# Optimization experiments

Measured on AMD Instinct MI355X. Metric: run time of the kernel, lower is better.

The kernel has to match this reference:

```python
import jax, jax.numpy as jnp
import numpy as np

U, I, H, E, EL = 100000, 50000, 128, 600000, 200000


def setup_inputs() -> dict:
    key = jax.random.key(0)
    ks = jax.random.split(key, 24)
    inp = {}
    inp["user_emb"] = jax.random.normal(ks[0], (U, H), jnp.float32) * 0.1
    inp["item_emb"] = jax.random.normal(ks[1], (I, H), jnp.float32) * 0.1
    s = 1.0 / np.sqrt(H)
    names = ["w1_ui_l", "w1_ui_r", "w1_iu_l", "w1_iu_r",
             "w2_ui_l", "w2_ui_r", "w2_iu_l", "w2_iu_r"]
    for i, n in enumerate(names):
        inp[n] = jax.random.uniform(ks[2 + i], (H, H), jnp.float32, -s, s)
    for i, n in enumerate(["b1_ui", "b1_iu", "b2_ui", "b2_iu"]):
        inp[n] = jax.random.uniform(ks[10 + i], (H,), jnp.float32, -s, s)
    inp["user_node_id"] = jnp.arange(U, dtype=jnp.int32)
    inp["item_node_id"] = jnp.arange(I, dtype=jnp.int32)
    src_u = jax.random.randint(ks[14], (E,), 0, U, jnp.int32)
    dst_i = jax.random.randint(ks[15], (E,), 0, I, jnp.int32)
    inp["edge_index_ui"] = jnp.stack([src_u, dst_i])  # user -> item
    inp["edge_index_iu"] = jnp.stack([dst_i, src_u])  # item -> user (reverse)
    lu = jax.random.randint(ks[16], (EL,), 0, U, jnp.int32)
    li = jax.random.randint(ks[17], (EL,), 0, I, jnp.int32)
    inp["edge_label_index"] = jnp.stack([lu, li])
    return inp


def _sage(x_src, x_dst, edge_index, w_l, b_l, w_r, num_dst):
    # PyG SAGEConv: out = lin_l(mean_j x_src[j]) + lin_r(x_dst)
    src, dst = edge_index[0], edge_index[1]
    msg = x_src[src]                                   # [E, H] gather
    agg = jax.ops.segment_sum(msg, dst, num_segments=num_dst)
    cnt = jax.ops.segment_sum(jnp.ones((msg.shape[0],), msg.dtype), dst,
                              num_segments=num_dst)
    mean = agg / jnp.maximum(cnt, 1.0)[:, None]
    return mean @ w_l + b_l + x_dst @ w_r


def reference(user_emb, item_emb,
              w1_ui_l, w1_ui_r, w1_iu_l, w1_iu_r,
              w2_ui_l, w2_ui_r, w2_iu_l, w2_iu_r,
              b1_ui, b1_iu, b2_ui, b2_iu,
              user_node_id, item_node_id,
              edge_index_ui, edge_index_iu, edge_label_index):
    xu = user_emb[user_node_id]   # [U, H]
    xi = item_emb[item_node_id]   # [I, H]
    # layer 1 (hetero: each dst type aggregates from its single incoming relation)
    u1 = jax.nn.relu(_sage(xi, xu, edge_index_iu, w1_iu_l, b1_iu, w1_iu_r, U))
    i1 = jax.nn.relu(_sage(xu, xi, edge_index_ui, w1_ui_l, b1_ui, w1_ui_r, I))
    # layer 2
    u2 = _sage(i1, u1, edge_index_iu, w2_iu_l, b2_iu, w2_iu_r, U)
    i2 = _sage(u1, i1, edge_index_ui, w2_ui_l, b2_ui, w2_ui_r, I)
    # edge-indexed dot-product classifier
    fu = u2[edge_label_index[0]]  # [EL, H]
    fi = i2[edge_label_index[1]]  # [EL, H]
    return jnp.sum(fu * fi, axis=-1)
```

## Files before the change

kernel.cpp:

```cpp
#include <hip/hip_runtime.h>
#include <hip/hip_bf16.h>
#include <cstdio>

#define U_N 100000
#define I_N 50000
#define H_DIM 128
#define E_N 600000
#define EL_N 200000

#define EPB 2048
#define NBLK ((E_N + EPB - 1) / EPB)
#define SH_U 8
#define SH_I 7
#define NB_U ((U_N + 255) >> 8)
#define NB_I ((I_N + 127) >> 7)
#define LH_U (NB_U * NBLK)
#define LH_I (NB_I * NBLK)
#define LH_TOT (LH_U + LH_I)

#define CVT_BLK (((U_N + I_N) * 16) / 256)
#define PREP_BLK 512
#define NBU2 ((U_N + 255) / 256)
#define NBI2 ((I_N + 255) / 256)

typedef __attribute__((ext_vector_type(8))) short bh8;
typedef __attribute__((ext_vector_type(4))) float f32x4;
typedef __attribute__((ext_vector_type(8))) unsigned short u16x8;

__device__ inline unsigned short f2b(float f) {
  unsigned u = __builtin_bit_cast(unsigned, f);
  u += 0x7fffu + ((u >> 16) & 1u);
  return (unsigned short)(u >> 16);
}
__device__ inline float b2f(unsigned short h) {
  unsigned u = ((unsigned)h) << 16;
  return __builtin_bit_cast(float, u);
}

__global__ __launch_bounds__(256) void prep_all(
    const float* __restrict__ xu, const float* __restrict__ xi,
    const int* __restrict__ unid, const int* __restrict__ inid,
    unsigned short* __restrict__ ub, unsigned short* __restrict__ ib,
    const float* __restrict__ l0, const float* __restrict__ r0, short* __restrict__ o0,
    const float* __restrict__ l1, const float* __restrict__ r1, short* __restrict__ o1,
    const float* __restrict__ l2, const float* __restrict__ r2, short* __restrict__ o2,
    const float* __restrict__ l3, const float* __restrict__ r3, short* __restrict__ o3,
    const int* __restrict__ e_ui, int* __restrict__ hist) {
  __shared__ int h[512];
  const int b = blockIdx.x;
  const int tid = threadIdx.x;
  if (b < CVT_BLK) {
    int t = b * 256 + tid;
    const float* x;
    unsigned short* xb;
    int row, seg;
    if (t < U_N * 16) {
      row = t >> 4; seg = t & 15;
      int r0_ = row;
      row = unid ? unid[row] : row;
      x = xu; xb = ub + (size_t)r0_ * H_DIM;
    } else {
      int t2 = t - U_N * 16;
      row = t2 >> 4; seg = t2 & 15;
      int r0_ = row;
      row = inid ? inid[row] : row;
      x = xi; xb = ib + (size_t)r0_ * H_DIM;
    }
    const float* p = x + (size_t)row * H_DIM + seg * 8;
    float4 a = ((const float4*)p)[0];
    float4 c = ((const float4*)p)[1];
    u16x8 v;
    v[0] = f2b(a.x); v[1] = f2b(a.y); v[2] = f2b(a.z); v[3] = f2b(a.w);
    v[4] = f2b(c.x); v[5] = f2b(c.y); v[6] = f2b(c.z); v[7] = f2b(c.w);
    *(u16x8*)(xb + seg * 8) = v;
  } else if (b < CVT_BLK + PREP_BLK) {
    int t = (b - CVT_BLK) * 256 + tid;
    int set = t >> 15, s = t & 32767;
    const float *wl, *wr; short* W2;
    if (set == 0)      { wl = l0; wr = r0; W2 = o0; }
    else if (set == 1) { wl = l1; wr = r1; W2 = o1; }
    else if (set == 2) { wl = l2; wr = r2; W2 = o2; }
    else               { wl = l3; wr = r3; W2 = o3; }
    int col = s >> 8, k = s & 255;
    float v = (k < 128) ? wl[k * 128 + col] : wr[(k - 128) * 128 + col];
    W2[col * 256 + k] = (short)f2b(v);
  } else {
    int hb = b - CVT_BLK - PREP_BLK;
    int side = hb >= NBLK;
    int blk = side ? hb - NBLK : hb;
    const int* dst = e_ui + (side ? E_N : 0);
    int shift = side ? SH_I : SH_U;
    int nbins = side ? NB_I : NB_U;
    int hbase = side ? LH_U : 0;
    for (int i = tid; i < nbins; i += 256) h[i] = 0;
    __syncthreads();
    const int base = blk * EPB;
    const int end = min(base + EPB, E_N);
    for (int i = base + tid; i < end; i += 256)
      atomicAdd(&h[((unsigned)dst[i]) >> shift], 1);
    __syncthreads();
    for (int i = tid; i < nbins; i += 256)
      hist[hbase + i * NBLK + blk] = h[i];
  }
}

__global__ __launch_bounds__(256) void scan_p1(const int* __restrict__ cnt,
                                               int* __restrict__ bsum, int n) {
  const int t = threadIdx.x;
  const int base = blockIdx.x * 1024 + t * 4;
  int s = 0;
  for (int j = 0; j < 4; ++j) {
    int i = base + j;
    if (i < n) s += cnt[i];
  }
  for (int off = 32; off > 0; off >>= 1) s += __shfl_down(s, off, 64);
  __shared__ int wsum[4];
  if ((t & 63) == 0) wsum[t >> 6] = s;
  __syncthreads();
  if (t == 0) bsum[blockIdx.x] = wsum[0] + wsum[1] + wsum[2] + wsum[3];
}

__global__ __launch_bounds__(256) void scan_p2(int* __restrict__ bsum, int nb) {
  __shared__ int sm[256];
  const int t = threadIdx.x;
  int v = (t < nb) ? bsum[t] : 0;
  sm[t] = v;
  __syncthreads();
  for (int d = 1; d < 256; d <<= 1) {
    int x = (t >= d) ? sm[t - d] : 0;
    __syncthreads();
    sm[t] += x;
    __syncthreads();
  }
  if (t < nb) bsum[t] = sm[t] - v;
}

__global__ __launch_bounds__(256) void scan_p3(const int* __restrict__ cnt,
                                               const int* __restrict__ bsum,
                                               int* __restrict__ off, int n) {
  const int t = threadIdx.x;
  const int lane = t & 63, wv = t >> 6;
  const int base = blockIdx.x * 1024 + t * 4;
  int vals[4];
  int s = 0;
  for (int j = 0; j < 4; ++j) {
    int i = base + j;
    vals[j] = (i < n) ? cnt[i] : 0;
    s += vals[j];
  }
  int inc = s;
  for (int d = 1; d < 64; d <<= 1) {
    int x = __shfl_up(inc, d, 64);
    if (lane >= d) inc += x;
  }
  __shared__ int wsum[4];
  if (lane == 63) wsum[wv] = inc;
  __syncthreads();
  int wbase = 0;
  for (int w = 0; w < wv; ++w) wbase += wsum[w];
  int excl = wbase + (inc - s) + bsum[blockIdx.x];
  for (int j = 0; j < 4; ++j) {
    int i = base + j;
    if (i < n) off[i] = excl;
    excl += vals[j];
  }
}

__global__ __launch_bounds__(256) void bin_scatter2(const int* __restrict__ e_ui,
                                                    const int* __restrict__ hoff,
                                                    unsigned* __restrict__ bucketed) {
  __shared__ int cur[512];
  const int t = threadIdx.x;
  const int hb = blockIdx.x;
  const int side = hb >= NBLK;
  const int blk = side ? hb - NBLK : hb;
  const int* dst = e_ui + (side ? E_N : 0);
  const int* src = e_ui + (side ? 0 : E_N);
  const int shift = side ? SH_I : SH_U;
  const int nbins = side ? NB_I : NB_U;
  const int hbase = side ? LH_U : 0;
  for (int i = t; i < nbins; i += 256) cur[i] = hoff[hbase + i * NBLK + blk];
  __syncthreads();
  const int base = blk * EPB;
  const int end = min(base + EPB, E_N);
  const unsigned mask = (1u << shift) - 1u;
  for (int i = base + t; i < end; i += 256) {
    unsigned d = (unsigned)dst[i];
    int bin = (int)(d >> shift);
    int pos = atomicAdd(&cur[bin], 1);
    bucketed[pos] = ((d & mask) << 24) | (unsigned)src[i];
  }
}

__global__ __launch_bounds__(256) void bin_group2(const int* __restrict__ hoff,
                                                  const unsigned* __restrict__ bucketed,
                                                  int* __restrict__ csr,
                                                  int* __restrict__ cnt_u,
                                                  int* __restrict__ off_u,
                                                  int* __restrict__ cnt_i,
                                                  int* __restrict__ off_i) {
  __shared__ int cl[256];
  __shared__ int cur[256];
  __shared__ int wsum[4];
  const int b = blockIdx.x;
  const int t = threadIdx.x;
  const int side = b >= NB_U;
  const int bb = side ? b - NB_U : b;
  const int shift = side ? SH_I : SH_U;
  const int N = side ? I_N : U_N;
  int* cnt = side ? cnt_i : cnt_u;
  int* off = side ? off_i : off_u;
  int start, end;
  if (!side) {
    start = hoff[bb * NBLK];
    end = (bb + 1 < NB_U) ? hoff[(bb + 1) * NBLK] : E_N;
  } else {
    start = hoff[LH_U + bb * NBLK];
    end = (bb + 1 < NB_I) ? hoff[LH_U + (bb + 1) * NBLK] : 2 * E_N;
  }
  const int ndst = 1 << shift;
  const int base = bb << shift;
  if (t < ndst) cl[t] = 0;
  __syncthreads();
  for (int i = start + t; i < end; i += 256)
    atomicAdd(&cl[bucketed[i] >> 24], 1);
  __syncthreads();
  int v = (t < ndst) ? cl[t] : 0;
  const int lane = t & 63, wv = t >> 6;
  int inc = v;
  for (int d = 1; d < 64; d <<= 1) {
    int x = __shfl_up(inc, d, 64);
    if (lane >= d) inc += x;
  }
  if (lane == 63) wsum[wv] = inc;
  __syncthreads();
  int wbase = 0;
  for (int q = 0; q < wv; ++q) wbase += wsum[q];
  int excl = wbase + inc - v;
  if (t < ndst) {
    cur[t] = start + excl;
    int node = base + t;
    if (node < N) { cnt[node] = v; off[node] = start + excl; }
  }
  __syncthreads();
  for (int i = start + t; i < end; i += 256) {
    unsigned w = bucketed[i];
    int pos = atomicAdd(&cur[w >> 24], 1);
    csr[pos] = (int)(w & 0xFFFFFFu);
  }
}

__global__ __launch_bounds__(256) void gather_mean2(
    const int* __restrict__ off_u, const int* __restrict__ cnt_u,
    const unsigned short* __restrict__ xsrc_u, unsigned short* __restrict__ agg_u,
    const int* __restrict__ off_i, const int* __restrict__ cnt_i,
    const unsigned short* __restrict__ xsrc_i, unsigned short* __restrict__ agg_i,
    const int* __restrict__ csr) {
  long t = (long)blockIdx.x * 256 + threadIdx.x;
  int node = (int)(t >> 4);
  int lane = (int)(t & 15);
  const int* off; const int* cnt;
  const unsigned short* xb; unsigned short* aggb;
  if (node < U_N) {
    off = off_u; cnt = cnt_u; xb = xsrc_u; aggb = agg_u;
  } else {
    node -= U_N;
    if (node >= I_N) return;
    off = off_i; cnt = cnt_i; xb = xsrc_i; aggb = agg_i;
  }
  int o = off[node], c = cnt[node];
  float acc[8] = {};
  for (int j0 = 0; j0 < c; j0 += 16) {
    int nj = c - j0;
    if (nj > 16) nj = 16;
    int sidx = (lane < nj) ? csr[o + j0 + lane] : 0;
    int j = 0;
    for (; j + 4 <= nj; j += 4) {
      u16x8 v0, v1, v2, v3;
      {
        int s0 = __shfl(sidx, j + 0, 16);
        int s1 = __shfl(sidx, j + 1, 16);
        int s2 = __shfl(sidx, j + 2, 16);
        int s3 = __shfl(sidx, j + 3, 16);
        v0 = *(const u16x8*)(xb + (size_t)s0 * H_DIM + lane * 8);
        v1 = *(const u16x8*)(xb + (size_t)s1 * H_DIM + lane * 8);
        v2 = *(const u16x8*)(xb + (size_t)s2 * H_DIM + lane * 8);
        v3 = *(const u16x8*)(xb + (size_t)s3 * H_DIM + lane * 8);
      }
      for (int k = 0; k < 8; ++k) acc[k] += b2f(v0[k]);
      for (int k = 0; k < 8; ++k) acc[k] += b2f(v1[k]);
      for (int k = 0; k < 8; ++k) acc[k] += b2f(v2[k]);
      for (int k = 0; k < 8; ++k) acc[k] += b2f(v3[k]);
    }
    for (; j < nj; ++j) {
      int s = __shfl(sidx, j, 16);
      u16x8 v = *(const u16x8*)(xb + (size_t)s * H_DIM + lane * 8);
      for (int k = 0; k < 8; ++k) acc[k] += b2f(v[k]);
    }
  }
  float inv = 1.0f / (float)(c > 0 ? c : 1);
  u16x8 r;
  for (int k = 0; k < 8; ++k) r[k] = f2b(acc[k] * inv);
  *(u16x8*)(aggb + (size_t)node * H_DIM + lane * 8) = r;
}

__global__ __launch_bounds__(256, 2) void sage_gemm2(
    const unsigned short* __restrict__ agg_u, const unsigned short* __restrict__ x_u,
    const short* __restrict__ W2_u, const float* __restrict__ bias_u,
    unsigned short* __restrict__ out_u,
    const unsigned short* __restrict__ agg_i, const unsigned short* __restrict__ x_i,
    const short* __restrict__ W2_i, const float* __restrict__ bias_i,
    unsigned short* __restrict__ out_i, int relu) {
  const unsigned short *aggb, *xb;
  const short* W2;
  const float* bias;
  unsigned short* outb;
  int N, blk;
  if (blockIdx.x < NBU2) {
    aggb = agg_u; xb = x_u; W2 = W2_u; bias = bias_u; outb = out_u;
    N = U_N; blk = blockIdx.x;
  } else {
    aggb = agg_i; xb = x_i; W2 = W2_i; bias = bias_i; outb = out_i;
    N = I_N; blk = blockIdx.x - NBU2;
  }

  __shared__ short wlds[128 * 256];
  const int tid = threadIdx.x;
  for (int c = tid; c < 4096; c += 256) {
    int col = c >> 5, g = c & 31;
    uint4 v = *(const uint4*)(W2 + col * 256 + g * 8);
    *(uint4*)(&wlds[col * 256 + ((g ^ (col & 15)) * 8)]) = v;
  }
  __syncthreads();

  const int lane = tid & 63;
  const int wave = tid >> 6;
  const int q = lane >> 4;
  const int n16 = lane & 15;
  const int rowbase = blk * 256 + wave * 64;

  const unsigned short* aptr[4];
  const unsigned short* xptr[4];
  for (int g = 0; g < 4; ++g) {
    int row = rowbase + g * 16 + n16;
    int rr = row < N ? row : 0;
    aptr[g] = aggb + (size_t)rr * H_DIM + q * 8;
    xptr[g] = xb + (size_t)rr * H_DIM + q * 8;
  }

  f32x4 acc[4][8] = {};

  for (int kt = 0; kt < 8; ++kt) {
    const int k0 = kt * 32;
    bh8 afrag[4];
    for (int g = 0; g < 4; ++g) {
      const unsigned short* p = (kt < 4) ? (aptr[g] + k0) : (xptr[g] + (k0 - 128));
      afrag[g] = *(const bh8*)(p);
    }
    const int swz = ((kt * 4 + q) ^ n16) * 8;
    for (int c = 0; c < 8; ++c) {
      bh8 b = *(const bh8*)(&wlds[(c * 16 + n16) * 256 + swz]);
      acc[0][c] = __builtin_amdgcn_mfma_f32_16x16x32_bf16(afrag[0], b, acc[0][c], 0, 0, 0);
      acc[1][c] = __builtin_amdgcn_mfma_f32_16x16x32_bf16(afrag[1], b, acc[1][c], 0, 0, 0);
      acc[2][c] = __builtin_amdgcn_mfma_f32_16x16x32_bf16(afrag[2], b, acc[2][c], 0, 0, 0);
      acc[3][c] = __builtin_amdgcn_mfma_f32_16x16x32_bf16(afrag[3], b, acc[3][c], 0, 0, 0);
    }
  }

  float bcol[8];
  for (int c = 0; c < 8; ++c) bcol[c] = bias[c * 16 + n16];

  for (int g = 0; g < 4; ++g) {
    for (int r = 0; r < 4; ++r) {
      int row = rowbase + g * 16 + q * 4 + r;
      if (row >= N) continue;
      for (int c = 0; c < 8; ++c) {
        float v = acc[g][c][r] + bcol[c];
        if (relu) v = v > 0.0f ? v : 0.0f;
        outb[(size_t)row * H_DIM + c * 16 + n16] = f2b(v);
      }
    }
  }
}

__global__ __launch_bounds__(256) void final_dot(const int* __restrict__ lbl,
                                                 const unsigned short* __restrict__ u2,
                                                 const unsigned short* __restrict__ i2,
                                                 float* __restrict__ out) {
  long t = (long)blockIdx.x * 256 + threadIdx.x;
  int e = (int)(t >> 4);
  if (e >= EL_N) return;
  int lane = (int)(t & 15);
  int lu = lbl[e];
  int li = lbl[EL_N + e];
  u16x8 a = *(const u16x8*)(u2 + (size_t)lu * H_DIM + lane * 8);
  u16x8 b = *(const u16x8*)(i2 + (size_t)li * H_DIM + lane * 8);
  float p = 0.f;
  for (int k = 0; k < 8; ++k) p += b2f(a[k]) * b2f(b[k]);
  for (int off = 8; off > 0; off >>= 1) p += __shfl_down(p, off, 16);
  if (lane == 0) out[e] = p;
}

extern "C" void kernel_launch(void* const* d_in, const int* in_sizes, int n_in,
                              void* d_out, int out_size, void* d_ws, size_t ws_size,
                              hipStream_t stream) {
  const float* user_emb = (const float*)d_in[0];
  const float* item_emb = (const float*)d_in[1];
  const float* w1_ui_l = (const float*)d_in[2];
  const float* w1_ui_r = (const float*)d_in[3];
  const float* w1_iu_l = (const float*)d_in[4];
  const float* w1_iu_r = (const float*)d_in[5];
  const float* w2_ui_l = (const float*)d_in[6];
  const float* w2_ui_r = (const float*)d_in[7];
  const float* w2_iu_l = (const float*)d_in[8];
  const float* w2_iu_r = (const float*)d_in[9];
  const float* b1_ui = (const float*)d_in[10];
  const float* b1_iu = (const float*)d_in[11];
  const float* b2_ui = (const float*)d_in[12];
  const float* b2_iu = (const float*)d_in[13];
  const int* unid = (const int*)d_in[14];
  const int* inid = (const int*)d_in[15];
  const int* e_ui = (const int*)d_in[16];
  const int* e_iu = (const int*)d_in[17];
  const int* elbl = (const int*)d_in[18];
  float* out = (float*)d_out;

  char* ws = (char*)d_ws;
  size_t o = 0;
  auto alloc = [&](size_t bytes) {
    char* p = ws + o;
    o = (o + bytes + 255) & ~(size_t)255;
    return p;
  };
  int* hist = (int*)alloc((size_t)LH_TOT * 4);
  int* hoff = (int*)alloc((size_t)LH_TOT * 4);
  unsigned* bkt = (unsigned*)alloc((size_t)2 * E_N * 4);
  int* csr = (int*)alloc((size_t)2 * E_N * 4);
  int* cnt_u = (int*)alloc((size_t)U_N * 4);
  int* cnt_i = (int*)alloc((size_t)I_N * 4);
  int* off_u = (int*)alloc((size_t)U_N * 4);
  int* off_i = (int*)alloc((size_t)I_N * 4);
  int* bsum = (int*)alloc(256 * 4);
  unsigned short* ue_b = (unsigned short*)alloc((size_t)U_N * H_DIM * 2);
  unsigned short* ie_b = (unsigned short*)alloc((size_t)I_N * H_DIM * 2);
  unsigned short* agg_u = (unsigned short*)alloc((size_t)U_N * H_DIM * 2);
  unsigned short* agg_i = (unsigned short*)alloc((size_t)I_N * H_DIM * 2);
  unsigned short* h1_u = (unsigned short*)alloc((size_t)U_N * H_DIM * 2);
  unsigned short* h1_i = (unsigned short*)alloc((size_t)I_N * H_DIM * 2);
  unsigned short* h2_u = (unsigned short*)alloc((size_t)U_N * H_DIM * 2);
  unsigned short* h2_i = (unsigned short*)alloc((size_t)I_N * H_DIM * 2);
  short* W2_1u = (short*)alloc(128 * 256 * 2);
  short* W2_1i = (short*)alloc(128 * 256 * 2);
  short* W2_2u = (short*)alloc(128 * 256 * 2);
  short* W2_2i = (short*)alloc(128 * 256 * 2);
  if (o > ws_size) {
    fprintf(stderr, "kernel_launch: ws too small, need %zu have %zu\n", o, ws_size);
    return;
  }

  prep_all<<<CVT_BLK + PREP_BLK + 2 * NBLK, 256, 0, stream>>>(
      user_emb, item_emb, unid, inid, ue_b, ie_b,
      w1_iu_l, w1_iu_r, W2_1u, w1_ui_l, w1_ui_r, W2_1i,
      w2_iu_l, w2_iu_r, W2_2u, w2_ui_l, w2_ui_r, W2_2i,
      e_ui, hist);

  const int nb1 = (LH_TOT + 1023) / 1024;
  scan_p1<<<nb1, 256, 0, stream>>>(hist, bsum, LH_TOT);
  scan_p2<<<1, 256, 0, stream>>>(bsum, nb1);
  scan_p3<<<nb1, 256, 0, stream>>>(hist, bsum, hoff, LH_TOT);

  bin_scatter2<<<2 * NBLK, 256, 0, stream>>>(e_ui, hoff, bkt);
  bin_group2<<<NB_U + NB_I, 256, 0, stream>>>(hoff, bkt, csr, cnt_u, off_u, cnt_i, off_i);

  const int g_blocks = ((U_N + I_N) * 16 + 255) / 256;
  gather_mean2<<<g_blocks, 256, 0, stream>>>(off_u, cnt_u, ie_b, agg_u,
                                             off_i, cnt_i, ue_b, agg_i, csr);
  sage_gemm2<<<NBU2 + NBI2, 256, 0, stream>>>(
      agg_u, ue_b, W2_1u, b1_iu, h1_u,
      agg_i, ie_b, W2_1i, b1_ui, h1_i, 1);

  gather_mean2<<<g_blocks, 256, 0, stream>>>(off_u, cnt_u, h1_i, agg_u,
                                             off_i, cnt_i, h1_u, agg_i, csr);
  sage_gemm2<<<NBU2 + NBI2, 256, 0, stream>>>(
      agg_u, h1_u, W2_2u, b2_iu, h2_u,
      agg_i, h1_i, W2_2i, b2_ui, h2_i, 0);

  final_dot<<<(EL_N * 16 + 255) / 256, 256, 0, stream>>>(elbl, h2_u, h2_i, out);
}
```

Baseline: 357.4 us.

## Fuse scan into single-pass chained scan; register-resident weights in SAGE GEMM

Replaces the three-kernel prefix scan with one decoupled chained-scan kernel. Each block waits on a flag/value from its predecessor, and the flags are zeroed inside prep_all. The SAGE GEMM drops its 64 KB LDS weight tile: each wave now holds its 32-column slice of the weights in registers, and every block handles 128 rows with all four waves sharing the same A rows. This removes two launches and the LDS staging and barrier, but it reloads the A fragments once per wave (4x the A global traffic). The chained scan also depends on blocks being scheduled in order for forward progress.

Measured after the change: 518.3 us. 45.0% more time.

```diff
diff --git a/kernel.cpp b/kernel.cpp
--- a/kernel.cpp
+++ b/kernel.cpp
@@ -17,11 +17,12 @@
 #define LH_U (NB_U * NBLK)
 #define LH_I (NB_I * NBLK)
 #define LH_TOT (LH_U + LH_I)
+#define SCAN_BLKS ((LH_TOT + 1023) / 1024)
 
 #define CVT_BLK (((U_N + I_N) * 16) / 256)
 #define PREP_BLK 512
-#define NBU2 ((U_N + 255) / 256)
-#define NBI2 ((I_N + 255) / 256)
+#define NBU3 ((U_N + 127) / 128)
+#define NBI3 ((I_N + 127) / 128)
 
 typedef __attribute__((ext_vector_type(8))) short bh8;
 typedef __attribute__((ext_vector_type(4))) float f32x4;
@@ -45,7 +46,7 @@
     const float* __restrict__ l1, const float* __restrict__ r1, short* __restrict__ o1,
     const float* __restrict__ l2, const float* __restrict__ r2, short* __restrict__ o2,
     const float* __restrict__ l3, const float* __restrict__ r3, short* __restrict__ o3,
-    const int* __restrict__ e_ui, int* __restrict__ hist) {
+    const int* __restrict__ e_ui, int* __restrict__ hist, int* __restrict__ fv) {
   __shared__ int h[512];
   const int b = blockIdx.x;
   const int tid = threadIdx.x;
@@ -86,6 +87,7 @@
     W2[col * 256 + k] = (short)f2b(v);
   } else {
     int hb = b - CVT_BLK - PREP_BLK;
+    if (hb == 0 && tid < SCAN_BLKS) fv[tid] = 0;
     int side = hb >= NBLK;
     int blk = side ? hb - NBLK : hb;
     const int* dst = e_ui + (side ? E_N : 0);
@@ -104,48 +106,18 @@
   }
 }
 
-__global__ __launch_bounds__(256) void scan_p1(const int* __restrict__ cnt,
-                                               int* __restrict__ bsum, int n) {
-  const int t = threadIdx.x;
-  const int base = blockIdx.x * 1024 + t * 4;
-  int s = 0;
-  for (int j = 0; j < 4; ++j) {
-    int i = base + j;
-    if (i < n) s += cnt[i];
-  }
-  for (int off = 32; off > 0; off >>= 1) s += __shfl_down(s, off, 64);
-  __shared__ int wsum[4];
-  if ((t & 63) == 0) wsum[t >> 6] = s;
-  __syncthreads();
-  if (t == 0) bsum[blockIdx.x] = wsum[0] + wsum[1] + wsum[2] + wsum[3];
-}
-
-__global__ __launch_bounds__(256) void scan_p2(int* __restrict__ bsum, int nb) {
-  __shared__ int sm[256];
-  const int t = threadIdx.x;
-  int v = (t < nb) ? bsum[t] : 0;
-  sm[t] = v;
-  __syncthreads();
-  for (int d = 1; d < 256; d <<= 1) {
-    int x = (t >= d) ? sm[t - d] : 0;
-    __syncthreads();
-    sm[t] += x;
-    __syncthreads();
-  }
-  if (t < nb) bsum[t] = sm[t] - v;
-}
-
-__global__ __launch_bounds__(256) void scan_p3(const int* __restrict__ cnt,
-                                               const int* __restrict__ bsum,
-                                               int* __restrict__ off, int n) {
+__global__ __launch_bounds__(256) void scan_chain(const int* __restrict__ hist,
+                                                  int* __restrict__ hoff,
+                                                  int* __restrict__ fv, int n) {
+  const int b = blockIdx.x;
   const int t = threadIdx.x;
   const int lane = t & 63, wv = t >> 6;
-  const int base = blockIdx.x * 1024 + t * 4;
+  const int base = b * 1024 + t * 4;
   int vals[4];
   int s = 0;
   for (int j = 0; j < 4; ++j) {
     int i = base + j;
-    vals[j] = (i < n) ? cnt[i] : 0;
+    vals[j] = (i < n) ? hist[i] : 0;
     s += vals[j];
   }
   int inc = s;
@@ -154,14 +126,27 @@
     if (lane >= d) inc += x;
   }
   __shared__ int wsum[4];
+  __shared__ int sprev;
   if (lane == 63) wsum[wv] = inc;
+  __syncthreads();
+  if (t == 0) {
+    int S = wsum[0] + wsum[1] + wsum[2] + wsum[3];
+    int prev = 0;
+    if (b > 0) {
+      int v;
+      do { v = atomicAdd(&fv[b - 1], 0); } while (v == 0);
+      prev = v - 1;
+    }
+    atomicExch(&fv[b], prev + S + 1);
+    sprev = prev;
+  }
   __syncthreads();
   int wbase = 0;
   for (int w = 0; w < wv; ++w) wbase += wsum[w];
-  int excl = wbase + (inc - s) + bsum[blockIdx.x];
+  int excl = sprev + wbase + (inc - s);
   for (int j = 0; j < 4; ++j) {
     int i = base + j;
-    if (i < n) off[i] = excl;
+    if (i < n) hoff[i] = excl;
     excl += vals[j];
   }
 }
@@ -304,7 +289,7 @@
   *(u16x8*)(aggb + (size_t)node * H_DIM + lane * 8) = r;
 }
 
-__global__ __launch_bounds__(256, 2) void sage_gemm2(
+__global__ __launch_bounds__(256) void sage_gemm3(
     const unsigned short* __restrict__ agg_u, const unsigned short* __restrict__ x_u,
     const short* __restrict__ W2_u, const float* __restrict__ bias_u,
     unsigned short* __restrict__ out_u,
@@ -316,68 +301,46 @@
   const float* bias;
   unsigned short* outb;
   int N, blk;
-  if (blockIdx.x < NBU2) {
+  if (blockIdx.x < NBU3) {
     aggb = agg_u; xb = x_u; W2 = W2_u; bias = bias_u; outb = out_u;
     N = U_N; blk = blockIdx.x;
   } else {
     aggb = agg_i; xb = x_i; W2 = W2_i; bias = bias_i; outb = out_i;
-    N = I_N; blk = blockIdx.x - NBU2;
-  }
-
-  __shared__ short wlds[128 * 256];
+    N = I_N; blk = blockIdx.x - NBU3;
+  }
   const int tid = threadIdx.x;
-  for (int c = tid; c < 4096; c += 256) {
-    int col = c >> 5, g = c & 31;
-    uint4 v = *(const uint4*)(W2 + col * 256 + g * 8);
-    *(uint4*)(&wlds[col * 256 + ((g ^ (col & 15)) * 8)]) = v;
-  }
-  __syncthreads();
-
-  const int lane = tid & 63;
-  const int wave = tid >> 6;
-  const int q = lane >> 4;
-  const int n16 = lane & 15;
-  const int rowbase = blk * 256 + wave * 64;
-
-  const unsigned short* aptr[4];
-  const unsigned short* xptr[4];
-  for (int g = 0; g < 4; ++g) {
+  const int lane = tid & 63, wave = tid >> 6;
+  const int n16 = lane & 15, q = lane >> 4;
+  const int rowbase = blk * 128;
+
+  bh8 bfrag[8][2];
+  for (int kt = 0; kt < 8; ++kt)
+    for (int j = 0; j < 2; ++j)
+      bfrag[kt][j] = *(const bh8*)(W2 + ((wave * 2 + j) * 16 + n16) * 256 + kt * 32 + q * 8);
+
+  float bc[2];
+  bc[0] = bias[(wave * 2 + 0) * 16 + n16];
+  bc[1] = bias[(wave * 2 + 1) * 16 + n16];
+
+  for (int g = 0; g < 8; ++g) {
     int row = rowbase + g * 16 + n16;
-    int rr = row < N ? row : 0;
-    aptr[g] = aggb + (size_t)rr * H_DIM + q * 8;
-    xptr[g] = xb + (size_t)rr * H_DIM + q * 8;
-  }
-
-  f32x4 acc[4][8] = {};
-
-  for (int kt = 0; kt < 8; ++kt) {
-    const int k0 = kt * 32;
-    bh8 afrag[4];
-    for (int g = 0; g < 4; ++g) {
-      const unsigned short* p = (kt < 4) ? (aptr[g] + k0) : (xptr[g] + (k0 - 128));
-      afrag[g] = *(const bh8*)(p);
-    }
-    const int swz = ((kt * 4 + q) ^ n16) * 8;
-    for (int c = 0; c < 8; ++c) {
-      bh8 b = *(const bh8*)(&wlds[(c * 16 + n16) * 256 + swz]);
-      acc[0][c] = __builtin_amdgcn_mfma_f32_16x16x32_bf16(afrag[0], b, acc[0][c], 0, 0, 0);
-      acc[1][c] = __builtin_amdgcn_mfma_f32_16x16x32_bf16(afrag[1], b, acc[1][c], 0, 0, 0);
-      acc[2][c] = __builtin_amdgcn_mfma_f32_16x16x32_bf16(afrag[2], b, acc[2][c], 0, 0, 0);
-      acc[3][c] = __builtin_amdgcn_mfma_f32_16x16x32_bf16(afrag[3], b, acc[3][c], 0, 0, 0);
-    }
-  }
-
-  float bcol[8];
-  for (int c = 0; c < 8; ++c) bcol[c] = bias[c * 16 + n16];
-
-  for (int g = 0; g < 4; ++g) {
+    int rr = row < N ? row : N - 1;
+    const unsigned short* ap = aggb + (size_t)rr * H_DIM + q * 8;
+    const unsigned short* xp = xb + (size_t)rr * H_DIM + q * 8;
+    f32x4 acc[2] = {};
+    for (int kt = 0; kt < 8; ++kt) {
+      const unsigned short* p = (kt < 4) ? (ap + kt * 32) : (xp + (kt - 4) * 32);
+      bh8 a = *(const bh8*)(p);
+      acc[0] = __builtin_amdgcn_mfma_f32_16x16x32_bf16(a, bfrag[kt][0], acc[0], 0, 0, 0);
+      acc[1] = __builtin_amdgcn_mfma_f32_16x16x32_bf16(a, bfrag[kt][1], acc[1], 0, 0, 0);
+    }
     for (int r = 0; r < 4; ++r) {
-      int row = rowbase + g * 16 + q * 4 + r;
-      if (row >= N) continue;
-      for (int c = 0; c < 8; ++c) {
-        float v = acc[g][c][r] + bcol[c];
+      int orow = rowbase + g * 16 + q * 4 + r;
+      if (orow >= N) continue;
+      for (int j = 0; j < 2; ++j) {
+        float v = acc[j][r] + bc[j];
         if (relu) v = v > 0.0f ? v : 0.0f;
-        outb[(size_t)row * H_DIM + c * 16 + n16] = f2b(v);
+        outb[(size_t)orow * H_DIM + (wave * 2 + j) * 16 + n16] = f2b(v);
       }
     }
   }
@@ -440,7 +403,7 @@
   int* cnt_i = (int*)alloc((size_t)I_N * 4);
   int* off_u = (int*)alloc((size_t)U_N * 4);
   int* off_i = (int*)alloc((size_t)I_N * 4);
-  int* bsum = (int*)alloc(256 * 4);
+  int* fv = (int*)alloc(SCAN_BLKS * 4);
   unsigned short* ue_b = (unsigned short*)alloc((size_t)U_N * H_DIM * 2);
   unsigned short* ie_b = (unsigned short*)alloc((size_t)I_N * H_DIM * 2);
   unsigned short* agg_u = (unsigned short*)alloc((size_t)U_N * H_DIM * 2);
@@ -462,12 +425,9 @@
       user_emb, item_emb, unid, inid, ue_b, ie_b,
       w1_iu_l, w1_iu_r, W2_1u, w1_ui_l, w1_ui_r, W2_1i,
       w2_iu_l, w2_iu_r, W2_2u, w2_ui_l, w2_ui_r, W2_2i,
-      e_ui, hist);
-
-  const int nb1 = (LH_TOT + 1023) / 1024;
-  scan_p1<<<nb1, 256, 0, stream>>>(hist, bsum, LH_TOT);
-  scan_p2<<<1, 256, 0, stream>>>(bsum, nb1);
-  scan_p3<<<nb1, 256, 0, stream>>>(hist, bsum, hoff, LH_TOT);
+      e_ui, hist, fv);
+
+  scan_chain<<<SCAN_BLKS, 256, 0, stream>>>(hist, hoff, fv, LH_TOT);
 
   bin_scatter2<<<2 * NBLK, 256, 0, stream>>>(e_ui, hoff, bkt);
   bin_group2<<<NB_U + NB_I, 256, 0, stream>>>(hoff, bkt, csr, cnt_u, off_u, cnt_i, off_i);
@@ -475,13 +435,13 @@
   const int g_blocks = ((U_N + I_N) * 16 + 255) / 256;
   gather_mean2<<<g_blocks, 256, 0, stream>>>(off_u, cnt_u, ie_b, agg_u,
                                              off_i, cnt_i, ue_b, agg_i, csr);
-  sage_gemm2<<<NBU2 + NBI2, 256, 0, stream>>>(
+  sage_gemm3<<<NBU3 + NBI3, 256, 0, stream>>>(
       agg_u, ue_b, W2_1u, b1_iu, h1_u,
       agg_i, ie_b, W2_1i, b1_ui, h1_i, 1);
 
   gather_mean2<<<g_blocks, 256, 0, stream>>>(off_u, cnt_u, h1_i, agg_u,
                                              off_i, cnt_i, h1_u, agg_i, csr);
-  sage_gemm2<<<NBU2 + NBI2, 256, 0, stream>>>(
+  sage_gemm3<<<NBU3 + NBI3, 256, 0, stream>>>(
       agg_u, h1_u, W2_2u, b2_iu, h2_u,
       agg_i, h1_i, W2_2i, b2_ui, h2_i, 0);
 
```
